# Kernel tuning notes

Hardware: AMD Instinct MI355X
Metric: run time of the kernel (lower is better)

## Reference

```python
import jax, jax.numpy as jnp
import numpy as np


def _ssm_layer(x, A, B, C, bias):
    # x: [Bt, T, D]; diagonal linear recurrence s_t = sigmoid(A)*s_{t-1} + B*x_t; y_t = C*s_t + bias
    a = jax.nn.sigmoid(A)

    def step(s, xt):
        s = a * s + B * xt
        return s, C * s + bias

    xT = jnp.swapaxes(x, 0, 1)  # [T, Bt, D]
    s0 = jnp.zeros(x.shape[::2], dtype=x.dtype)  # [Bt, D]
    _, yT = jax.lax.scan(step, s0, xT)
    return jnp.swapaxes(yT, 0, 1)  # [Bt, T, D]


def setup_inputs() -> dict:
    key = jax.random.key(0)
    ks = jax.random.split(key, 6)
    Bt, T, F, H, L = 8, 4096, 512, 1024, 4
    x = jax.random.normal(ks[0], (Bt, T, F), dtype=jnp.float32)
    W_in = jax.random.normal(ks[1], (F, H), dtype=jnp.float32) * (1.0 / np.sqrt(F))
    b_in = jnp.zeros((H,), dtype=jnp.float32)
    A = jax.random.uniform(ks[2], (L, H), dtype=jnp.float32)  # torch.rand init
    B = jax.random.normal(ks[3], (L, H), dtype=jnp.float32)
    C = jax.random.normal(ks[4], (L, H), dtype=jnp.float32)
    bias = jnp.zeros((L, H), dtype=jnp.float32)
    return {"x": x, "W_in": W_in, "b_in": b_in, "A": A, "B": B, "C": C, "bias": bias}


def reference(x, W_in, b_in, A, B, C, bias):
    # in_proj (dropout is identity at p=0)
    y = jnp.einsum('btf,fh->bth', x, W_in) + b_in
    n_layers = A.shape[0]
    for l in range(n_layers):  # small fixed layer count
        y = _ssm_layer(y, A[l], B[l], C[l], bias[l])
    # return_sequence=True, unidirectional -> y: [B, T, H]
    return y
```

## Files before the change

kernel.cpp:

```cpp
#include <hip/hip_runtime.h>
#include <hip/hip_bf16.h>
#include <stdint.h>

#define BT     8
#define T_SEQ  4096
#define K_F    512
#define N_H    1024
#define M_TOT  (BT * T_SEQ)
#define NLAYER 4
#define LC     32
#define NC     (T_SEQ / LC)

typedef short  bf16x8 __attribute__((ext_vector_type(8)));
typedef float  f32x4  __attribute__((ext_vector_type(4)));
typedef ushort u16x8  __attribute__((ext_vector_type(8)));
typedef ushort u16x4  __attribute__((ext_vector_type(4)));

__device__ __forceinline__ ushort f2bf(float f) {
  uint32_t u = __builtin_bit_cast(uint32_t, f);
  u += 0x7fffu + ((u >> 16) & 1u);
  return (ushort)(u >> 16);
}
__device__ __forceinline__ float bf2f(ushort u) {
  uint32_t x = (uint32_t)u << 16;
  return __builtin_bit_cast(float, x);
}

__device__ __forceinline__ void gload16(const void* g, void* l) {
  __builtin_amdgcn_global_load_lds(
      (const __attribute__((address_space(1))) uint32_t*)g,
      (__attribute__((address_space(3))) uint32_t*)l, 16, 0, 0);
}

__global__ __launch_bounds__(256) void cvt_x_kernel(const float* __restrict__ x,
                                                    ushort* __restrict__ xb) {
  const int i = blockIdx.x * 256 + threadIdx.x;
  const float4* xv = (const float4*)x;
  float4 v0 = xv[2 * i + 0];
  float4 v1 = xv[2 * i + 1];
  u16x8 o;
  o[0] = f2bf(v0.x); o[1] = f2bf(v0.y); o[2] = f2bf(v0.z); o[3] = f2bf(v0.w);
  o[4] = f2bf(v1.x); o[5] = f2bf(v1.y); o[6] = f2bf(v1.z); o[7] = f2bf(v1.w);
  *((u16x8*)xb + i) = o;
}

__global__ __launch_bounds__(256) void trans_w_kernel(const float* __restrict__ W,
                                                      ushort* __restrict__ Wt) {
  __shared__ float tile[32][33];
  const int lx = threadIdx.x & 31;
  const int ly = threadIdx.x >> 5;
  const int k0 = blockIdx.x * 32;
  const int n0 = blockIdx.y * 32;
#pragma unroll
  for (int j = 0; j < 32; j += 8)
    tile[ly + j][lx] = W[(size_t)(k0 + ly + j) * N_H + n0 + lx];
  __syncthreads();
#pragma unroll
  for (int j = 0; j < 32; j += 8)
    Wt[(size_t)(n0 + ly + j) * K_F + k0 + lx] = f2bf(tile[lx][ly + j]);
}

#define BM 128
#define BN 128
#define BKK 64

__global__ __launch_bounds__(256) void gemm_kernel(const ushort* __restrict__ Xb,
                                                   const ushort* __restrict__ Wt,
                                                   const float* __restrict__ bias,
                                                   ushort* __restrict__ Yb) {
  __shared__ ushort lds[BM * BKK * 2];
  ushort* lsA = lds;
  ushort* lsB = lds + BM * BKK;
  const int tid  = threadIdx.x;
  const int lane = tid & 63;
  const int wv   = tid >> 6;
  const int wr   = wv >> 1;
  const int wc   = wv & 1;
  const int m0   = blockIdx.x * BM;
  const int n0   = blockIdx.y * BN;

  const int srow = (lane >> 3);
  const int scol = (lane & 7) * 8;
  const ushort* gA = Xb + (size_t)m0 * K_F + scol;
  const ushort* gB = Wt + (size_t)n0 * K_F + scol;

  f32x4 acc[4][4];
#pragma unroll
  for (int i = 0; i < 4; i++)
#pragma unroll
    for (int j = 0; j < 4; j++) acc[i][j] = (f32x4)0.0f;

  const int lr = lane & 15;
  const int kg = (lane >> 4) * 8;

  for (int kt = 0; kt < K_F; kt += BKK) {
#pragma unroll
    for (int i = 0; i < 4; i++) {
      const int reg = wv * 4 + i;
      const int r   = reg * 8 + srow;
      gload16(gA + (size_t)r * K_F + kt, &lsA[reg * 512]);
      gload16(gB + (size_t)r * K_F + kt, &lsB[reg * 512]);
    }
    __syncthreads();

    bf16x8 af[4][2], bfr[4][2];
#pragma unroll
    for (int fm = 0; fm < 4; fm++)
#pragma unroll
      for (int kk = 0; kk < 2; kk++)
        af[fm][kk] = *(const bf16x8*)&lsA[(wr * 64 + fm * 16 + lr) * BKK + kk * 32 + kg];
#pragma unroll
    for (int fn = 0; fn < 4; fn++)
#pragma unroll
      for (int kk = 0; kk < 2; kk++)
        bfr[fn][kk] = *(const bf16x8*)&lsB[(wc * 64 + fn * 16 + lr) * BKK + kk * 32 + kg];

#pragma unroll
    for (int kk = 0; kk < 2; kk++)
#pragma unroll
      for (int fm = 0; fm < 4; fm++)
#pragma unroll
        for (int fn = 0; fn < 4; fn++)
          acc[fm][fn] = __builtin_amdgcn_mfma_f32_16x16x32_bf16(af[fm][kk], bfr[fn][kk],
                                                                acc[fm][fn], 0, 0, 0);
    __syncthreads();
  }

#pragma unroll
  for (int fn = 0; fn < 4; fn++) {
    const int col = wc * 64 + fn * 16 + lr;
    const float bv = bias[n0 + col];
#pragma unroll
    for (int fm = 0; fm < 4; fm++) {
      const int row0 = wr * 64 + fm * 16 + (lane >> 4) * 4;
#pragma unroll
      for (int i = 0; i < 4; i++)
        lds[(row0 + i) * BN + col] = f2bf(acc[fm][fn][i] + bv);
    }
  }
  __syncthreads();

  const int erow = tid >> 4;
  const int ecol = (tid & 15) * 8;
#pragma unroll
  for (int p = 0; p < 8; p++) {
    const int row = p * 16 + erow;
    u16x8 v = *(const u16x8*)&lds[row * BN + ecol];
    *(u16x8*)&Yb[(size_t)(m0 + row) * N_H + n0 + ecol] = v;
  }
}


__global__ __launch_bounds__(256) void chunk_state_kernel(
    const ushort* __restrict__ Yb, const float* __restrict__ A,
    const float* __restrict__ B, const float* __restrict__ C,
    const float* __restrict__ D, float* __restrict__ E) {
  const int b  = blockIdx.x / NC;
  const int c  = blockIdx.x % NC;
  const int h4 = threadIdx.x << 2;

  float a[4][4], bb[4][4], cc[4][4], dd[4][4];
#pragma unroll
  for (int l = 0; l < 4; l++) {
    f32x4 av = *(const f32x4*)(A + l * N_H + h4);
    f32x4 bv = *(const f32x4*)(B + l * N_H + h4);
    f32x4 cv = *(const f32x4*)(C + l * N_H + h4);
    f32x4 dv = *(const f32x4*)(D + l * N_H + h4);
#pragma unroll
    for (int ch = 0; ch < 4; ch++) {
      a[l][ch]  = 1.f / (1.f + __expf(-av[ch]));
      bb[l][ch] = bv[ch]; cc[l][ch] = cv[ch]; dd[l][ch] = dv[ch];
    }
  }

  float s[4][4] = {};
  const ushort* ybase = Yb + ((size_t)b * T_SEQ + (size_t)c * LC) * N_H + h4;
#pragma unroll 4
  for (int t = 0; t < LC; t++) {
    u16x4 xv = *(const u16x4*)(ybase + (size_t)t * N_H);
#pragma unroll
    for (int ch = 0; ch < 4; ch++) {
      float x = bf2f(xv[ch]);
#pragma unroll
      for (int l = 0; l < 4; l++) {
        s[l][ch] = fmaf(a[l][ch], s[l][ch], bb[l][ch] * x);
        x = fmaf(cc[l][ch], s[l][ch], dd[l][ch]);
      }
    }
  }

  f32x4* ep = (f32x4*)E + (size_t)(b * NC + c) * N_H + h4;
#pragma unroll
  for (int ch = 0; ch < 4; ch++) {
    f32x4 e;
    e[0] = s[0][ch]; e[1] = s[1][ch]; e[2] = s[2][ch]; e[3] = s[3][ch];
    ep[ch] = e;
  }
}

__global__ __launch_bounds__(256) void chunk_scan_kernel(
    const float* __restrict__ A, const float* __restrict__ B,
    const float* __restrict__ C, const float* __restrict__ E,
    float* __restrict__ S) {
  const int idx = blockIdx.x * 256 + threadIdx.x;
  const int b = idx >> 10;
  const int h = idx & (N_H - 1);

  float a[4], bcoef[4], ccoef[4];
#pragma unroll
  for (int l = 0; l < 4; l++) {
    a[l] = 1.f / (1.f + __expf(-A[l * N_H + h]));
    bcoef[l] = B[l * N_H + h];
    ccoef[l] = C[l * N_H + h];
  }

  float m[4][4] = {};
  m[0][0] = a[0];
  m[1][0] = bcoef[1] * ccoef[0] * a[0];
  m[1][1] = a[1];
  m[2][0] = bcoef[2] * ccoef[1] * m[1][0];
  m[2][1] = bcoef[2] * ccoef[1] * a[1];
  m[2][2] = a[2];
  m[3][0] = bcoef[3] * ccoef[2] * m[2][0];
  m[3][1] = bcoef[3] * ccoef[2] * m[2][1];
  m[3][2] = bcoef[3] * ccoef[2] * a[2];
  m[3][3] = a[3];

#pragma unroll
  for (int it = 0; it < 5; it++) {
    float t[4][4];
#pragma unroll
    for (int i = 0; i < 4; i++)
#pragma unroll
      for (int j = 0; j < 4; j++) {
        float acc = 0.f;
#pragma unroll
        for (int k = 0; k < 4; k++) acc = fmaf(m[i][k], m[k][j], acc);
        t[i][j] = acc;
      }
#pragma unroll
    for (int i = 0; i < 4; i++)
#pragma unroll
      for (int j = 0; j < 4; j++) m[i][j] = t[i][j];
  }

  float s[4] = {0.f, 0.f, 0.f, 0.f};
  const f32x4* Ep = (const f32x4*)E + (size_t)b * NC * N_H + h;
  f32x4* Sp = (f32x4*)S + (size_t)b * NC * N_H + h;
#pragma unroll 4
  for (int c = 0; c < NC; c++) {
    f32x4 sv;
    sv[0] = s[0]; sv[1] = s[1]; sv[2] = s[2]; sv[3] = s[3];
    Sp[(size_t)c * N_H] = sv;
    f32x4 e = Ep[(size_t)c * N_H];
    float ns[4];
#pragma unroll
    for (int i = 0; i < 4; i++) {
      float acc = e[i];
#pragma unroll
      for (int k = 0; k < 4; k++) acc = fmaf(m[i][k], s[k], acc);
      ns[i] = acc;
    }
#pragma unroll
    for (int i = 0; i < 4; i++) s[i] = ns[i];
  }
}

__global__ __launch_bounds__(256) void chunk_apply_kernel(
    const ushort* __restrict__ Yb, float* __restrict__ out,
    const float* __restrict__ A, const float* __restrict__ B,
    const float* __restrict__ C, const float* __restrict__ D,
    const float* __restrict__ S) {
  const int b  = blockIdx.x / NC;
  const int c  = blockIdx.x % NC;
  const int h4 = threadIdx.x << 2;

  float a[4][4], bb[4][4], cc[4][4], dd[4][4];
#pragma unroll
  for (int l = 0; l < 4; l++) {
    f32x4 av = *(const f32x4*)(A + l * N_H + h4);
    f32x4 bv = *(const f32x4*)(B + l * N_H + h4);
    f32x4 cv = *(const f32x4*)(C + l * N_H + h4);
    f32x4 dv = *(const f32x4*)(D + l * N_H + h4);
#pragma unroll
    for (int ch = 0; ch < 4; ch++) {
      a[l][ch]  = 1.f / (1.f + __expf(-av[ch]));
      bb[l][ch] = bv[ch]; cc[l][ch] = cv[ch]; dd[l][ch] = dv[ch];
    }
  }

  float s[4][4];
  const f32x4* sp = (const f32x4*)S + (size_t)(b * NC + c) * N_H + h4;
#pragma unroll
  for (int ch = 0; ch < 4; ch++) {
    f32x4 sv = sp[ch];
    s[0][ch] = sv[0]; s[1][ch] = sv[1]; s[2][ch] = sv[2]; s[3][ch] = sv[3];
  }

  const ushort* ybase = Yb + ((size_t)b * T_SEQ + (size_t)c * LC) * N_H + h4;
  f32x4* op = (f32x4*)(out + ((size_t)b * T_SEQ + (size_t)c * LC) * N_H) + (h4 >> 2);
#pragma unroll 4
  for (int t = 0; t < LC; t++) {
    u16x4 xv = *(const u16x4*)(ybase + (size_t)t * N_H);
    f32x4 ov;
#pragma unroll
    for (int ch = 0; ch < 4; ch++) {
      float x = bf2f(xv[ch]);
#pragma unroll
      for (int l = 0; l < 4; l++) {
        s[l][ch] = fmaf(a[l][ch], s[l][ch], bb[l][ch] * x);
        x = fmaf(cc[l][ch], s[l][ch], dd[l][ch]);
      }
      ov[ch] = x;
    }
    op[(size_t)t * (N_H / 4)] = ov;
  }
}

extern "C" void kernel_launch(void* const* d_in, const int* in_sizes, int n_in,
                              void* d_out, int out_size, void* d_ws, size_t ws_size,
                              hipStream_t stream) {
  const float* x    = (const float*)d_in[0];
  const float* W    = (const float*)d_in[1];
  const float* b_in = (const float*)d_in[2];
  const float* A    = (const float*)d_in[3];
  const float* B    = (const float*)d_in[4];
  const float* C    = (const float*)d_in[5];
  const float* bias = (const float*)d_in[6];
  float* out = (float*)d_out;

  char* wsb = (char*)d_ws;
  ushort* xb = (ushort*)wsb;
  ushort* Wt = (ushort*)(wsb + (size_t)33 * 1024 * 1024 - (size_t)N_H * K_F * 2);
  ushort* Yb = (ushort*)(wsb + (size_t)40 * 1024 * 1024);
  float*  E  = (float*)(wsb + (size_t)112 * 1024 * 1024);
  float*  S  = E + (size_t)BT * NC * N_H * 4;

  cvt_x_kernel<<<(M_TOT * K_F) / (256 * 8), 256, 0, stream>>>(x, xb);
  trans_w_kernel<<<dim3(K_F / 32, N_H / 32), 256, 0, stream>>>(W, Wt);
  gemm_kernel<<<dim3(M_TOT / BM, N_H / BN), 256, 0, stream>>>(xb, Wt, b_in, Yb);
  chunk_state_kernel<<<BT * NC, 256, 0, stream>>>(Yb, A, B, C, bias, E);
  chunk_scan_kernel<<<(BT * N_H) / 256, 256, 0, stream>>>(A, B, C, E, S);
  chunk_apply_kernel<<<BT * NC, 256, 0, stream>>>(Yb, out, A, B, C, bias, S);
}
```

Before: 168.9 us.

## Fuse chunk-state computation into GEMM epilogue and merge prep kernels

The chunk-local SSM state pass now runs in the GEMM epilogue, reading the bf16 output tile still held in LDS instead of re-reading Yb from global memory in a separate kernel. The x conversion and W transpose kernels are merged into one launch. This removes a full pass over Yb and two launches, but adds a serial 32-step recurrence per thread to the GEMM blocks, which lengthens their tail.

```diff
diff --git a/kernel.cpp b/kernel.cpp
--- a/kernel.cpp
+++ b/kernel.cpp
@@ -32,42 +32,49 @@
       (__attribute__((address_space(3))) uint32_t*)l, 16, 0, 0);
 }
 
-__global__ __launch_bounds__(256) void cvt_x_kernel(const float* __restrict__ x,
-                                                    ushort* __restrict__ xb) {
-  const int i = blockIdx.x * 256 + threadIdx.x;
-  const float4* xv = (const float4*)x;
-  float4 v0 = xv[2 * i + 0];
-  float4 v1 = xv[2 * i + 1];
-  u16x8 o;
-  o[0] = f2bf(v0.x); o[1] = f2bf(v0.y); o[2] = f2bf(v0.z); o[3] = f2bf(v0.w);
-  o[4] = f2bf(v1.x); o[5] = f2bf(v1.y); o[6] = f2bf(v1.z); o[7] = f2bf(v1.w);
-  *((u16x8*)xb + i) = o;
-}
-
-__global__ __launch_bounds__(256) void trans_w_kernel(const float* __restrict__ W,
-                                                      ushort* __restrict__ Wt) {
+#define CVT_BLOCKS ((M_TOT * K_F) / (256 * 8))
+
+__global__ __launch_bounds__(256) void prep_kernel(const float* __restrict__ x,
+                                                   ushort* __restrict__ xb,
+                                                   const float* __restrict__ W,
+                                                   ushort* __restrict__ Wt) {
   __shared__ float tile[32][33];
-  const int lx = threadIdx.x & 31;
-  const int ly = threadIdx.x >> 5;
-  const int k0 = blockIdx.x * 32;
-  const int n0 = blockIdx.y * 32;
-#pragma unroll
-  for (int j = 0; j < 32; j += 8)
-    tile[ly + j][lx] = W[(size_t)(k0 + ly + j) * N_H + n0 + lx];
-  __syncthreads();
-#pragma unroll
-  for (int j = 0; j < 32; j += 8)
-    Wt[(size_t)(n0 + ly + j) * K_F + k0 + lx] = f2bf(tile[lx][ly + j]);
+  const int bid = blockIdx.x;
+  if (bid < CVT_BLOCKS) {
+    const int i = bid * 256 + threadIdx.x;
+    const float4* xv = (const float4*)x;
+    float4 v0 = xv[2 * i + 0];
+    float4 v1 = xv[2 * i + 1];
+    u16x8 o;
+    o[0] = f2bf(v0.x); o[1] = f2bf(v0.y); o[2] = f2bf(v0.z); o[3] = f2bf(v0.w);
+    o[4] = f2bf(v1.x); o[5] = f2bf(v1.y); o[6] = f2bf(v1.z); o[7] = f2bf(v1.w);
+    *((u16x8*)xb + i) = o;
+  } else {
+    const int idx = bid - CVT_BLOCKS;
+    const int k0 = (idx & 15) * 32;
+    const int n0 = (idx >> 4) * 32;
+    const int lx = threadIdx.x & 31;
+    const int ly = threadIdx.x >> 5;
+#pragma unroll
+    for (int j = 0; j < 32; j += 8)
+      tile[ly + j][lx] = W[(size_t)(k0 + ly + j) * N_H + n0 + lx];
+    __syncthreads();
+#pragma unroll
+    for (int j = 0; j < 32; j += 8)
+      Wt[(size_t)(n0 + ly + j) * K_F + k0 + lx] = f2bf(tile[lx][ly + j]);
+  }
 }
 
 #define BM 128
 #define BN 128
 #define BKK 64
 
-__global__ __launch_bounds__(256) void gemm_kernel(const ushort* __restrict__ Xb,
-                                                   const ushort* __restrict__ Wt,
-                                                   const float* __restrict__ bias,
-                                                   ushort* __restrict__ Yb) {
+__global__ __launch_bounds__(256) void gemm_kernel(
+    const ushort* __restrict__ Xb, const ushort* __restrict__ Wt,
+    const float* __restrict__ bias, ushort* __restrict__ Yb,
+    const float* __restrict__ As, const float* __restrict__ Bs,
+    const float* __restrict__ Cs, const float* __restrict__ Ds,
+    float* __restrict__ E) {
   __shared__ ushort lds[BM * BKK * 2];
   ushort* lsA = lds;
   ushort* lsB = lds + BM * BKK;
@@ -148,53 +155,40 @@
     u16x8 v = *(const u16x8*)&lds[row * BN + ecol];
     *(u16x8*)&Yb[(size_t)(m0 + row) * N_H + n0 + ecol] = v;
   }
-}
-
-
-__global__ __launch_bounds__(256) void chunk_state_kernel(
-    const ushort* __restrict__ Yb, const float* __restrict__ A,
-    const float* __restrict__ B, const float* __restrict__ C,
-    const float* __restrict__ D, float* __restrict__ E) {
-  const int b  = blockIdx.x / NC;
-  const int c  = blockIdx.x % NC;
-  const int h4 = threadIdx.x << 2;
-
-  float a[4][4], bb[4][4], cc[4][4], dd[4][4];
-#pragma unroll
-  for (int l = 0; l < 4; l++) {
-    f32x4 av = *(const f32x4*)(A + l * N_H + h4);
-    f32x4 bv = *(const f32x4*)(B + l * N_H + h4);
-    f32x4 cv = *(const f32x4*)(C + l * N_H + h4);
-    f32x4 dv = *(const f32x4*)(D + l * N_H + h4);
-#pragma unroll
-    for (int ch = 0; ch < 4; ch++) {
-      a[l][ch]  = 1.f / (1.f + __expf(-av[ch]));
-      bb[l][ch] = bv[ch]; cc[l][ch] = cv[ch]; dd[l][ch] = dv[ch];
-    }
-  }
-
-  float s[4][4] = {};
-  const ushort* ybase = Yb + ((size_t)b * T_SEQ + (size_t)c * LC) * N_H + h4;
+
+  {
+    const int bidx = m0 >> 12;
+    const int c0   = (m0 & (T_SEQ - 1)) >> 5;
+    const int hl   = tid & 127;
+    const int ck0  = tid >> 7;
+    const int h    = n0 + hl;
+
+    float a[4], bb[4], cc[4], dd[4];
+#pragma unroll
+    for (int l = 0; l < 4; l++) {
+      a[l]  = 1.f / (1.f + __expf(-As[l * N_H + h]));
+      bb[l] = Bs[l * N_H + h];
+      cc[l] = Cs[l * N_H + h];
+      dd[l] = Ds[l * N_H + h];
+    }
+
+#pragma unroll
+    for (int p = 0; p < 2; p++) {
+      const int ck = ck0 + p * 2;
+      float s[4] = {0.f, 0.f, 0.f, 0.f};
 #pragma unroll 4
-  for (int t = 0; t < LC; t++) {
-    u16x4 xv = *(const u16x4*)(ybase + (size_t)t * N_H);
-#pragma unroll
-    for (int ch = 0; ch < 4; ch++) {
-      float x = bf2f(xv[ch]);
-#pragma unroll
-      for (int l = 0; l < 4; l++) {
-        s[l][ch] = fmaf(a[l][ch], s[l][ch], bb[l][ch] * x);
-        x = fmaf(cc[l][ch], s[l][ch], dd[l][ch]);
+      for (int t = 0; t < LC; t++) {
+        float xv = bf2f(lds[(ck * LC + t) * BN + hl]);
+#pragma unroll
+        for (int l = 0; l < 4; l++) {
+          s[l] = fmaf(a[l], s[l], bb[l] * xv);
+          xv = fmaf(cc[l], s[l], dd[l]);
+        }
       }
-    }
-  }
-
-  f32x4* ep = (f32x4*)E + (size_t)(b * NC + c) * N_H + h4;
-#pragma unroll
-  for (int ch = 0; ch < 4; ch++) {
-    f32x4 e;
-    e[0] = s[0][ch]; e[1] = s[1][ch]; e[2] = s[2][ch]; e[3] = s[3][ch];
-    ep[ch] = e;
+      f32x4 e;
+      e[0] = s[0]; e[1] = s[1]; e[2] = s[2]; e[3] = s[3];
+      ((f32x4*)E)[(size_t)(bidx * NC + c0 + ck) * N_H + h] = e;
+    }
   }
 }
 
@@ -336,10 +330,9 @@
   float*  E  = (float*)(wsb + (size_t)112 * 1024 * 1024);
   float*  S  = E + (size_t)BT * NC * N_H * 4;
 
-  cvt_x_kernel<<<(M_TOT * K_F) / (256 * 8), 256, 0, stream>>>(x, xb);
-  trans_w_kernel<<<dim3(K_F / 32, N_H / 32), 256, 0, stream>>>(W, Wt);
-  gemm_kernel<<<dim3(M_TOT / BM, N_H / BN), 256, 0, stream>>>(xb, Wt, b_in, Yb);
-  chunk_state_kernel<<<BT * NC, 256, 0, stream>>>(Yb, A, B, C, bias, E);
+  prep_kernel<<<CVT_BLOCKS + 512, 256, 0, stream>>>(x, xb, W, Wt);
+  gemm_kernel<<<dim3(M_TOT / BM, N_H / BN), 256, 0, stream>>>(xb, Wt, b_in, Yb,
+                                                              A, B, C, bias, E);
   chunk_scan_kernel<<<(BT * N_H) / 256, 256, 0, stream>>>(A, B, C, E, S);
   chunk_apply_kernel<<<BT * NC, 256, 0, stream>>>(Yb, out, A, B, C, bias, S);
 }
```

Result: faster. 157.3 us (-6.9%).
